# Kernel tuning notes

Measured on AMD Instinct MI355X. Metric: run time of the kernel, lower is better.

## Reference

```python
import jax, jax.numpy as jnp
import numpy as np

N_EMBD = 1024
N_HEAD = 16
HEAD_SIZE = 64


def setup_inputs() -> dict:
    key = jax.random.key(0)
    ks = jax.random.split(key, 6)
    B, T, C, H, D = 2, 2048, N_EMBD, N_HEAD, HEAD_SIZE
    s = 1.0 / np.sqrt(C)
    x = jax.random.normal(ks[0], (B, T, C), dtype=jnp.float32)
    Wq = jax.random.normal(ks[1], (H, C, D), dtype=jnp.float32) * s
    Wk = jax.random.normal(ks[2], (H, C, D), dtype=jnp.float32) * s
    Wv = jax.random.normal(ks[3], (H, C, D), dtype=jnp.float32) * s
    Wo = jax.random.normal(ks[4], (H * D, C), dtype=jnp.float32) * (1.0 / np.sqrt(H * D))
    bo = jax.random.normal(ks[5], (C,), dtype=jnp.float32) * 0.01
    return {"x": x, "Wq": Wq, "Wk": Wk, "Wv": Wv, "Wo": Wo, "bo": bo}


def reference(x, Wq, Wk, Wv, Wo, bo):
    B, T, C = x.shape
    H, _, D = Wq.shape
    # Per-head projections, batched across heads: [B,H,T,D]
    q = jnp.einsum('btc,hcd->bhtd', x, Wq)
    k = jnp.einsum('btc,hcd->bhtd', x, Wk)
    v = jnp.einsum('btc,hcd->bhtd', x, Wv)
    # NOTE: original scales by sqrt(C) = sqrt(n_embd), not sqrt(head_size)
    scale = 1.0 / jnp.sqrt(jnp.float32(C))
    att = jnp.einsum('bhtd,bhsd->bhts', q, k) * scale  # [B,H,T,T]
    causal = jnp.tril(jnp.ones((T, T), dtype=bool))
    att = jnp.where(causal, att, -jnp.inf)
    att = jax.nn.softmax(att, axis=-1)
    # dropout omitted (eval mode / deterministic reference)
    out = jnp.einsum('bhts,bhsd->bhtd', att, v)  # [B,H,T,D]
    out = out.transpose(0, 2, 1, 3).reshape(B, T, H * D)
    return out @ Wo + bo
```

## Files before the change

### kernel.cpp

```cpp
#include <hip/hip_runtime.h>
#include <hip/hip_bf16.h>


typedef __hip_bfloat16 bf16;
typedef __bf16 v8bf __attribute__((ext_vector_type(8)));
typedef float  v4f  __attribute__((ext_vector_type(4)));
typedef unsigned long long u64;
typedef unsigned int u32;

#define MFMA16(a, b, c) __builtin_amdgcn_mfma_f32_16x16x32_bf16((a), (b), (c), 0, 0, 0)

__device__ __forceinline__ bf16 f2b(float x) { return __float2bfloat16(x); }
__device__ __forceinline__ __bf16 f2braw(float x) {
  bf16 t = __float2bfloat16(x);
  return *reinterpret_cast<__bf16*>(&t);
}
__device__ __forceinline__ unsigned short f2bu(float x) {
  bf16 t = __float2bfloat16(x);
  return *reinterpret_cast<unsigned short*>(&t);
}

__device__ __forceinline__ void load16_lds(const bf16* gptr, const bf16* lptr) {
  __builtin_amdgcn_global_load_lds(
      (const __attribute__((address_space(1))) u32*)gptr,
      (__attribute__((address_space(3))) u32*)lptr, 16, 0, 0);
}

__global__ __launch_bounds__(256) void prep_kernel(
    const float* __restrict__ x,
    const float* __restrict__ Wq, const float* __restrict__ Wk,
    const float* __restrict__ Wv, const float* __restrict__ Wo,
    bf16* __restrict__ xb, bf16* __restrict__ wt, bf16* __restrict__ wot)
{
  __shared__ float Lt[32][33];
  const int bid = blockIdx.x, tid = threadIdx.x;

  if (bid < 2048) {
    size_t i = ((size_t)bid * 256 + tid) * 8;
    float4 f0 = *(const float4*)(x + i);
    float4 f1 = *(const float4*)(x + i + 4);
    v8bf v;
    v[0] = f2braw(f0.x); v[1] = f2braw(f0.y); v[2] = f2braw(f0.z); v[3] = f2braw(f0.w);
    v[4] = f2braw(f1.x); v[5] = f2braw(f1.y); v[6] = f2braw(f1.z); v[7] = f2braw(f1.w);
    *(v8bf*)(xb + i) = v;
    return;
  }
  const int tx = tid & 31, ty = tid >> 5;
  if (bid < 5120) {
    const int idx = bid - 2048;
    const int z = idx >> 6, rem = idx & 63;
    const int p = z >> 4, h = z & 15;
    const float* ib = ((p == 0) ? Wq : (p == 1) ? Wk : Wv) + (size_t)h * 65536;
    bf16* ob = wt + (size_t)z * 65536;
    const int j0 = (rem & 1) * 32, i0 = (rem >> 1) * 32;
    #pragma unroll
    for (int r = 0; r < 4; ++r)
      Lt[ty + 8 * r][tx] = ib[(size_t)(i0 + ty + 8 * r) * 64 + j0 + tx];
    __syncthreads();
    #pragma unroll
    for (int r = 0; r < 4; ++r)
      ob[(size_t)(j0 + ty + 8 * r) * 1024 + i0 + tx] = f2b(Lt[tx][ty + 8 * r]);
  } else {
    const int idx = bid - 5120;
    const int j0 = (idx & 31) * 32, i0 = (idx >> 5) * 32;
    #pragma unroll
    for (int r = 0; r < 4; ++r)
      Lt[ty + 8 * r][tx] = Wo[(size_t)(i0 + ty + 8 * r) * 1024 + j0 + tx];
    __syncthreads();
    #pragma unroll
    for (int r = 0; r < 4; ++r)
      wot[(size_t)(j0 + ty + 8 * r) * 1024 + i0 + tx] = f2b(Lt[tx][ty + 8 * r]);
  }
}

__global__ __launch_bounds__(256) void qkv_gemm_kernel(
    const bf16* __restrict__ xb, const bf16* __restrict__ wt,
    bf16* __restrict__ qkv)
{
  __shared__ __align__(16) bf16 Ash[2][128][32];
  __shared__ __align__(16) bf16 Bsh[2][128][32];

  const int mt = blockIdx.x, nt = blockIdx.y;
  const int tid = threadIdx.x, w = tid >> 6, lane = tid & 63;
  const int ln = lane & 15, quad = lane >> 4;
  const int wm = w >> 1, wn = w & 1;
  const int m0 = mt * 128, n0 = nt * 128;

  const v4f vzero = {0.f, 0.f, 0.f, 0.f};
  v4f acc[4][4];
  #pragma unroll
  for (int mf = 0; mf < 4; ++mf)
    #pragma unroll
    for (int nf = 0; nf < 4; ++nf) acc[mf][nf] = vzero;

  const int srow = lane >> 2, sseg = (lane & 3) * 8;
  const bf16* ga = xb + (size_t)(m0 + 32 * w + srow) * 1024 + sseg;
  const bf16* gb = wt + (size_t)(n0 + 32 * w + srow) * 1024 + sseg;

  {
    load16_lds(ga,             &Ash[0][32 * w][0]);
    load16_lds(ga + 16 * 1024, &Ash[0][32 * w + 16][0]);
    load16_lds(gb,             &Bsh[0][32 * w][0]);
    load16_lds(gb + 16 * 1024, &Bsh[0][32 * w + 16][0]);
  }

  for (int kt = 0; kt < 32; ++kt) {
    const int buf = kt & 1;
    __syncthreads();

    v8bf af[4], bfv[4];
    #pragma unroll
    for (int mf = 0; mf < 4; ++mf)
      af[mf] = *(const v8bf*)&Ash[buf][wm * 64 + mf * 16 + ln][quad * 8];
    #pragma unroll
    for (int nf = 0; nf < 4; ++nf)
      bfv[nf] = *(const v8bf*)&Bsh[buf][wn * 64 + nf * 16 + ln][quad * 8];

    if (kt < 31) {
      const int k0 = (kt + 1) * 32, nb = buf ^ 1;
      load16_lds(ga + k0,             &Ash[nb][32 * w][0]);
      load16_lds(ga + 16 * 1024 + k0, &Ash[nb][32 * w + 16][0]);
      load16_lds(gb + k0,             &Bsh[nb][32 * w][0]);
      load16_lds(gb + 16 * 1024 + k0, &Bsh[nb][32 * w + 16][0]);
    }

    #pragma unroll
    for (int mf = 0; mf < 4; ++mf)
      #pragma unroll
      for (int nf = 0; nf < 4; ++nf)
        acc[mf][nf] = MFMA16(af[mf], bfv[nf], acc[mf][nf]);
  }

  const int jcol0 = n0 + wn * 64;
  const int p = jcol0 >> 10;
  const int h = (jcol0 >> 6) & 15;
  const float scale = (p == 0) ? 0.0450841149f : 1.0f;

  if (p < 2) {
    bf16* base = qkv + (size_t)p * 4194304 + (size_t)h * 262144;
    #pragma unroll
    for (int mf = 0; mf < 4; ++mf)
      #pragma unroll
      for (int nf = 0; nf < 4; ++nf) {
        int d = nf * 16 + ln;
        #pragma unroll
        for (int r = 0; r < 4; ++r) {
          int m = m0 + wm * 64 + mf * 16 + quad * 4 + r;
          base[(size_t)m * 64 + d] = f2b(acc[mf][nf][r] * scale);
        }
      }
  } else {
    bf16* vb = qkv + (size_t)2 * 4194304 + (size_t)h * 262144;
    #pragma unroll
    for (int mf = 0; mf < 4; ++mf) {
      int mrow = m0 + wm * 64 + mf * 16 + quad * 4;
      int bi = mrow >> 11, t0 = mrow & 2047;
      #pragma unroll
      for (int nf = 0; nf < 4; ++nf) {
        int d = nf * 16 + ln;
        u64 pk = (u64)f2bu(acc[mf][nf][0]) |
                 ((u64)f2bu(acc[mf][nf][1]) << 16) |
                 ((u64)f2bu(acc[mf][nf][2]) << 32) |
                 ((u64)f2bu(acc[mf][nf][3]) << 48);
        *(u64*)(vb + (size_t)bi * 131072 + (size_t)d * 2048 + t0) = pk;
      }
    }
  }
}

__global__ __launch_bounds__(256, 4) void attn_kernel(
    const bf16* __restrict__ qkv, bf16* __restrict__ att)
{
  __shared__ __align__(16) bf16 Ksh[2][64][64];
  __shared__ __align__(16) bf16 Vsh[2][64][64];

  const int fid = blockIdx.x;
  const int j = fid >> 5;
  const int jr = j & 7, jq = j >> 3;
  const int mt = (jq == 0) ? (31 - jr) : (jq == 1) ? (8 + jr)
               : (jq == 2) ? (23 - jr) : jr;
  const int grp = fid & 31;
  const int b = grp >> 4, h = grp & 15;

  const int tid = threadIdx.x, w = tid >> 6, lane = tid & 63;
  const int ln = lane & 15, quad = lane >> 4;

  const bf16* qbase  = qkv + (size_t)h * 262144 + (size_t)b * 131072;
  const bf16* kbase  = qbase + 4194304;
  const bf16* vtbase = qbase + 8388608;

  const int l8 = lane & 7, r8 = lane >> 3;
  const int slot = l8 ^ r8;
  const int p0 = w * 16 + r8, p1 = p0 + 8;
  const int kp0 = (p0 & 32) | ((p0 & 12) << 1) | ((p0 & 16) >> 2) | (p0 & 3);
  const int kp1 = (p1 & 32) | ((p1 & 12) << 1) | ((p1 & 16) >> 2) | (p1 & 3);
  const bf16* gk0 = kbase + kp0 * 64 + slot * 8;
  const bf16* gk1 = kbase + kp1 * 64 + slot * 8;
  const bf16* gv0 = vtbase + p0 * 2048 + slot * 8;
  const bf16* gv1 = gv0 + 8 * 2048;

  const int sw = ln & 7;
  const int c0 = ((quad    ) ^ sw) * 8;
  const int c1 = ((quad + 4) ^ sw) * 8;
  const int rowoff = ln * 64;

  v8bf vone;
  {
    unsigned short u = 0x3F80;
    __bf16 e = *reinterpret_cast<__bf16*>(&u);
    #pragma unroll
    for (int jj = 0; jj < 8; ++jj) vone[jj] = e;
  }
  const v4f vzero = {0.f, 0.f, 0.f, 0.f};
  const float NEG = -30000.0f;

  #define STAGE(KB, BUF) {                                       \
    load16_lds(gk0 + (KB) * 4096, &Ksh[BUF][w * 16][0]);         \
    load16_lds(gk1 + (KB) * 4096, &Ksh[BUF][w * 16 + 8][0]);     \
    load16_lds(gv0 + (KB) * 64,   &Vsh[BUF][w * 16][0]);         \
    load16_lds(gv1 + (KB) * 64,   &Vsh[BUF][w * 16 + 8][0]); }

  const int wrow = mt * 64 + w * 16;
  const int qg = wrow + ln;

  v8bf aq[2];
  #pragma unroll
  for (int ks = 0; ks < 2; ++ks)
    aq[ks] = *(const v8bf*)(qbase + (size_t)(wrow + ln) * 64 + ks * 32 + quad * 8);

  v4f o[4], lacc;
  lacc = vzero;
  #pragma unroll
  for (int dt = 0; dt < 4; ++dt) o[dt] = vzero;

  STAGE(0, 0)

  const int kb_end = mt;
  for (int kb = 0; kb <= kb_end; ++kb) {
    const int buf = kb & 1;
    __syncthreads();

    v8bf kf[2][4], vf[2][4];
    const bf16* kr = &Ksh[buf][0][0];
    const bf16* vr = &Vsh[buf][0][0];
    #pragma unroll
    for (int nf = 0; nf < 4; ++nf) {
      kf[0][nf] = *(const v8bf*)(kr + nf * 1024 + rowoff + c0);
      kf[1][nf] = *(const v8bf*)(kr + nf * 1024 + rowoff + c1);
      vf[0][nf] = *(const v8bf*)(vr + nf * 1024 + rowoff + c0);
      vf[1][nf] = *(const v8bf*)(vr + nf * 1024 + rowoff + c1);
    }

    if (kb < kb_end) STAGE(kb + 1, buf ^ 1)

    __builtin_amdgcn_s_setprio(1);
    v4f s[4];
    #pragma unroll
    for (int nf = 0; nf < 4; ++nf) s[nf] = vzero;
    #pragma unroll
    for (int ks = 0; ks < 2; ++ks)
      #pragma unroll
      for (int nf = 0; nf < 4; ++nf)
        s[nf] = MFMA16(kf[ks][nf], aq[ks], s[nf]);
    __builtin_amdgcn_s_setprio(0);

    if (kb == kb_end) {
      #pragma unroll
      for (int nf = 0; nf < 4; ++nf) {
        const int kc = kb * 64 + (nf >> 1) * 32 + quad * 8 + (nf & 1) * 4;
        #pragma unroll
        for (int r = 0; r < 4; ++r)
          if (kc + r > qg) s[nf][r] = NEG;
      }
    }

    float ex[4][4];
    #pragma unroll
    for (int nf = 0; nf < 4; ++nf)
      #pragma unroll
      for (int r = 0; r < 4; ++r)
        ex[nf][r] = exp2f(s[nf][r]);

    union { u32 w[4]; v8bf v; } pu[2];
    #pragma unroll
    for (int ks = 0; ks < 2; ++ks)
      #pragma unroll
      for (int hh = 0; hh < 2; ++hh)
        #pragma unroll
        for (int wi = 0; wi < 2; ++wi)
          asm("v_cvt_pk_bf16_f32 %0, %1, %2"
              : "=v"(pu[ks].w[hh * 2 + wi])
              : "v"(ex[2 * ks + hh][2 * wi]), "v"(ex[2 * ks + hh][2 * wi + 1]));

    __builtin_amdgcn_s_setprio(1);
    lacc = MFMA16(pu[0].v, vone, lacc);
    lacc = MFMA16(pu[1].v, vone, lacc);
    #pragma unroll
    for (int ks = 0; ks < 2; ++ks)
      #pragma unroll
      for (int dt = 0; dt < 4; ++dt)
        o[dt] = MFMA16(pu[ks].v, vf[ks][dt], o[dt]);
    __builtin_amdgcn_s_setprio(0);
  }
  #undef STAGE

  v4f inv;
  #pragma unroll
  for (int r = 0; r < 4; ++r) inv[r] = 1.0f / lacc[r];
  #pragma unroll
  for (int dt = 0; dt < 4; ++dt)
    #pragma unroll
    for (int r = 0; r < 4; ++r) {
      int m = b * 2048 + wrow + quad * 4 + r;
      att[(size_t)m * 1024 + h * 64 + dt * 16 + ln] = f2b(o[dt][r] * inv[r]);
    }
}

__global__ __launch_bounds__(256) void out_gemm_kernel(
    const bf16* __restrict__ att, const bf16* __restrict__ wot,
    const float* __restrict__ bo, float* __restrict__ out)
{
  __shared__ __align__(16) bf16 Ash[2][128][32];
  __shared__ __align__(16) bf16 Bsh[2][64][32];

  const int mt = blockIdx.x, nt = blockIdx.y;
  const int tid = threadIdx.x, w = tid >> 6, lane = tid & 63;
  const int ln = lane & 15, quad = lane >> 4;
  const int wm = w >> 1, wn = w & 1;
  const int m0 = mt * 128, n0 = nt * 64;

  const v4f vzero = {0.f, 0.f, 0.f, 0.f};
  v4f acc[4][2];
  #pragma unroll
  for (int mf = 0; mf < 4; ++mf)
    #pragma unroll
    for (int nf = 0; nf < 2; ++nf) acc[mf][nf] = vzero;

  const int srow = lane >> 2, sseg = (lane & 3) * 8;
  const bf16* ga = att + (size_t)(m0 + 32 * w + srow) * 1024 + sseg;
  const bf16* gb = wot + (size_t)(n0 + 16 * w + srow) * 1024 + sseg;

  {
    load16_lds(ga,             &Ash[0][32 * w][0]);
    load16_lds(ga + 16 * 1024, &Ash[0][32 * w + 16][0]);
    load16_lds(gb,             &Bsh[0][16 * w][0]);
  }

  for (int kt = 0; kt < 32; ++kt) {
    const int buf = kt & 1;
    __syncthreads();

    v8bf af[4], bfv[2];
    #pragma unroll
    for (int mf = 0; mf < 4; ++mf)
      af[mf] = *(const v8bf*)&Ash[buf][wm * 64 + mf * 16 + ln][quad * 8];
    #pragma unroll
    for (int nf = 0; nf < 2; ++nf)
      bfv[nf] = *(const v8bf*)&Bsh[buf][wn * 32 + nf * 16 + ln][quad * 8];

    if (kt < 31) {
      const int k0 = (kt + 1) * 32, nb = buf ^ 1;
      load16_lds(ga + k0,             &Ash[nb][32 * w][0]);
      load16_lds(ga + 16 * 1024 + k0, &Ash[nb][32 * w + 16][0]);
      load16_lds(gb + k0,             &Bsh[nb][16 * w][0]);
    }

    #pragma unroll
    for (int mf = 0; mf < 4; ++mf)
      #pragma unroll
      for (int nf = 0; nf < 2; ++nf)
        acc[mf][nf] = MFMA16(af[mf], bfv[nf], acc[mf][nf]);
  }

  #pragma unroll
  for (int nf = 0; nf < 2; ++nf) {
    int j = n0 + wn * 32 + nf * 16 + ln;
    float bias = bo[j];
    #pragma unroll
    for (int mf = 0; mf < 4; ++mf)
      #pragma unroll
      for (int r = 0; r < 4; ++r) {
        int m = m0 + wm * 64 + mf * 16 + quad * 4 + r;
        out[(size_t)m * 1024 + j] = acc[mf][nf][r] + bias;
      }
  }
}

extern "C" void kernel_launch(void* const* d_in, const int* in_sizes, int n_in,
                              void* d_out, int out_size, void* d_ws, size_t ws_size,
                              hipStream_t stream) {
  const float* x  = (const float*)d_in[0];
  const float* Wq = (const float*)d_in[1];
  const float* Wk = (const float*)d_in[2];
  const float* Wv = (const float*)d_in[3];
  const float* Wo = (const float*)d_in[4];
  const float* bo = (const float*)d_in[5];
  float* out = (float*)d_out;

  bf16* xb  = (bf16*)d_ws;
  bf16* wt  = xb + 4194304;
  bf16* wot = xb + 7340032;
  bf16* qkv = xb + 8388608;
  bf16* att = xb + 20971520;

  prep_kernel<<<6144, 256, 0, stream>>>(x, Wq, Wk, Wv, Wo, xb, wt, wot);
  qkv_gemm_kernel<<<dim3(32, 24), 256, 0, stream>>>(xb, wt, qkv);
  attn_kernel<<<1024, 256, 0, stream>>>(qkv, att);
  out_gemm_kernel<<<dim3(32, 16), 256, 0, stream>>>(att, wot, bo, out);
}
```

Measured before the change: 168.7 us.

## Split attention key tile across wave pairs with LDS reduction of partial outputs

Changes the attention kernel's wave decomposition. Each wave now handles 32 query rows against half of each 64-key tile, instead of 16 query rows against the full tile. Each wave therefore loads half the K fragments and reuses its K and V fragments across two query chunks, which cuts LDS read traffic per MFMA. The partial outputs and row sums from the two key halves are combined at the end through an LDS union buffer, at the cost of an extra reduction phase, two more barriers and more accumulator registers.

```diff
diff --git a/kernel.cpp b/kernel.cpp
--- a/kernel.cpp
+++ b/kernel.cpp
@@ -171,8 +171,11 @@
 __global__ __launch_bounds__(256, 4) void attn_kernel(
     const bf16* __restrict__ qkv, bf16* __restrict__ att)
 {
-  __shared__ __align__(16) bf16 Ksh[2][64][64];
-  __shared__ __align__(16) bf16 Vsh[2][64][64];
+  union ShU {
+    struct { bf16 K[2][64][64]; bf16 V[2][64][64]; } t;
+    struct { float O[2][64][36]; float L[2][36]; } c;
+  };
+  __shared__ __align__(16) ShU sh;
 
   const int fid = blockIdx.x;
   const int j = fid >> 5;
@@ -184,6 +187,7 @@
 
   const int tid = threadIdx.x, w = tid >> 6, lane = tid & 63;
   const int ln = lane & 15, quad = lane >> 4;
+  const int qh = w & 1, kh = w >> 1;
 
   const bf16* qbase  = qkv + (size_t)h * 262144 + (size_t)b * 131072;
   const bf16* kbase  = qbase + 4194304;
@@ -200,9 +204,11 @@
   const bf16* gv1 = gv0 + 8 * 2048;
 
   const int sw = ln & 7;
-  const int c0 = ((quad    ) ^ sw) * 8;
-  const int c1 = ((quad + 4) ^ sw) * 8;
-  const int rowoff = ln * 64;
+  const int cc0 = ((quad    ) ^ sw) * 8;
+  const int cc1 = ((quad + 4) ^ sw) * 8;
+  const int cck = kh ? cc1 : cc0;
+  const int krow0 = (kh * 32 + ln) * 64;
+  const int krow1 = krow0 + 16 * 64;
 
   v8bf vone;
   {
@@ -215,23 +221,29 @@
   const float NEG = -30000.0f;
 
   #define STAGE(KB, BUF) {                                       \
-    load16_lds(gk0 + (KB) * 4096, &Ksh[BUF][w * 16][0]);         \
-    load16_lds(gk1 + (KB) * 4096, &Ksh[BUF][w * 16 + 8][0]);     \
-    load16_lds(gv0 + (KB) * 64,   &Vsh[BUF][w * 16][0]);         \
-    load16_lds(gv1 + (KB) * 64,   &Vsh[BUF][w * 16 + 8][0]); }
-
-  const int wrow = mt * 64 + w * 16;
-  const int qg = wrow + ln;
-
-  v8bf aq[2];
+    load16_lds(gk0 + (KB) * 4096, &sh.t.K[BUF][w * 16][0]);      \
+    load16_lds(gk1 + (KB) * 4096, &sh.t.K[BUF][w * 16 + 8][0]);  \
+    load16_lds(gv0 + (KB) * 64,   &sh.t.V[BUF][w * 16][0]);      \
+    load16_lds(gv1 + (KB) * 64,   &sh.t.V[BUF][w * 16 + 8][0]); }
+
+  const int row0 = mt * 64;
+  const int qrow = row0 + qh * 32;
+
+  v8bf aq[2][2];
   #pragma unroll
-  for (int ks = 0; ks < 2; ++ks)
-    aq[ks] = *(const v8bf*)(qbase + (size_t)(wrow + ln) * 64 + ks * 32 + quad * 8);
-
-  v4f o[4], lacc;
-  lacc = vzero;
+  for (int mc = 0; mc < 2; ++mc)
+    #pragma unroll
+    for (int ks = 0; ks < 2; ++ks)
+      aq[mc][ks] = *(const v8bf*)(qbase +
+          (size_t)(qrow + mc * 16 + ln) * 64 + ks * 32 + quad * 8);
+
+  v4f o[2][4], lacc[2];
   #pragma unroll
-  for (int dt = 0; dt < 4; ++dt) o[dt] = vzero;
+  for (int mc = 0; mc < 2; ++mc) {
+    lacc[mc] = vzero;
+    #pragma unroll
+    for (int dt = 0; dt < 4; ++dt) o[mc][dt] = vzero;
+  }
 
   STAGE(0, 0)
 
@@ -240,80 +252,99 @@
     const int buf = kb & 1;
     __syncthreads();
 
-    v8bf kf[2][4], vf[2][4];
-    const bf16* kr = &Ksh[buf][0][0];
-    const bf16* vr = &Vsh[buf][0][0];
-    #pragma unroll
-    for (int nf = 0; nf < 4; ++nf) {
-      kf[0][nf] = *(const v8bf*)(kr + nf * 1024 + rowoff + c0);
-      kf[1][nf] = *(const v8bf*)(kr + nf * 1024 + rowoff + c1);
-      vf[0][nf] = *(const v8bf*)(vr + nf * 1024 + rowoff + c0);
-      vf[1][nf] = *(const v8bf*)(vr + nf * 1024 + rowoff + c1);
-    }
+    v8bf kf[2][2], vf[4];
+    const bf16* kr = &sh.t.K[buf][0][0];
+    const bf16* vr = &sh.t.V[buf][0][0];
+    kf[0][0] = *(const v8bf*)(kr + krow0 + cc0);
+    kf[1][0] = *(const v8bf*)(kr + krow0 + cc1);
+    kf[0][1] = *(const v8bf*)(kr + krow1 + cc0);
+    kf[1][1] = *(const v8bf*)(kr + krow1 + cc1);
+    #pragma unroll
+    for (int dt = 0; dt < 4; ++dt)
+      vf[dt] = *(const v8bf*)(vr + (dt * 16 + ln) * 64 + cck);
 
     if (kb < kb_end) STAGE(kb + 1, buf ^ 1)
 
-    __builtin_amdgcn_s_setprio(1);
-    v4f s[4];
-    #pragma unroll
-    for (int nf = 0; nf < 4; ++nf) s[nf] = vzero;
-    #pragma unroll
-    for (int ks = 0; ks < 2; ++ks)
-      #pragma unroll
-      for (int nf = 0; nf < 4; ++nf)
-        s[nf] = MFMA16(kf[ks][nf], aq[ks], s[nf]);
-    __builtin_amdgcn_s_setprio(0);
-
-    if (kb == kb_end) {
-      #pragma unroll
-      for (int nf = 0; nf < 4; ++nf) {
-        const int kc = kb * 64 + (nf >> 1) * 32 + quad * 8 + (nf & 1) * 4;
+    #pragma unroll
+    for (int mc = 0; mc < 2; ++mc) {
+      __builtin_amdgcn_s_setprio(1);
+      v4f s[2];
+      s[0] = vzero; s[1] = vzero;
+      #pragma unroll
+      for (int ks = 0; ks < 2; ++ks)
+        #pragma unroll
+        for (int nfl = 0; nfl < 2; ++nfl)
+          s[nfl] = MFMA16(kf[ks][nfl], aq[mc][ks], s[nfl]);
+      __builtin_amdgcn_s_setprio(0);
+
+      const int qg = qrow + mc * 16 + ln;
+      if (kb == kb_end) {
+        #pragma unroll
+        for (int nfl = 0; nfl < 2; ++nfl) {
+          const int kc = kb * 64 + kh * 32 + quad * 8 + nfl * 4;
+          #pragma unroll
+          for (int r = 0; r < 4; ++r)
+            if (kc + r > qg) s[nfl][r] = NEG;
+        }
+      }
+
+      float ex[2][4];
+      #pragma unroll
+      for (int nfl = 0; nfl < 2; ++nfl)
         #pragma unroll
         for (int r = 0; r < 4; ++r)
-          if (kc + r > qg) s[nf][r] = NEG;
-      }
-    }
-
-    float ex[4][4];
-    #pragma unroll
-    for (int nf = 0; nf < 4; ++nf)
-      #pragma unroll
-      for (int r = 0; r < 4; ++r)
-        ex[nf][r] = exp2f(s[nf][r]);
-
-    union { u32 w[4]; v8bf v; } pu[2];
-    #pragma unroll
-    for (int ks = 0; ks < 2; ++ks)
-      #pragma unroll
-      for (int hh = 0; hh < 2; ++hh)
+          ex[nfl][r] = exp2f(s[nfl][r]);
+
+      union { u32 uw[4]; v8bf v; } pu;
+      #pragma unroll
+      for (int nfl = 0; nfl < 2; ++nfl)
         #pragma unroll
         for (int wi = 0; wi < 2; ++wi)
           asm("v_cvt_pk_bf16_f32 %0, %1, %2"
-              : "=v"(pu[ks].w[hh * 2 + wi])
-              : "v"(ex[2 * ks + hh][2 * wi]), "v"(ex[2 * ks + hh][2 * wi + 1]));
-
-    __builtin_amdgcn_s_setprio(1);
-    lacc = MFMA16(pu[0].v, vone, lacc);
-    lacc = MFMA16(pu[1].v, vone, lacc);
-    #pragma unroll
-    for (int ks = 0; ks < 2; ++ks)
+              : "=v"(pu.uw[nfl * 2 + wi])
+              : "v"(ex[nfl][2 * wi]), "v"(ex[nfl][2 * wi + 1]));
+
+      __builtin_amdgcn_s_setprio(1);
+      lacc[mc] = MFMA16(pu.v, vone, lacc[mc]);
       #pragma unroll
       for (int dt = 0; dt < 4; ++dt)
-        o[dt] = MFMA16(pu[ks].v, vf[ks][dt], o[dt]);
-    __builtin_amdgcn_s_setprio(0);
+        o[mc][dt] = MFMA16(pu.v, vf[dt], o[mc][dt]);
+      __builtin_amdgcn_s_setprio(0);
+    }
   }
   #undef STAGE
 
-  v4f inv;
-  #pragma unroll
-  for (int r = 0; r < 4; ++r) inv[r] = 1.0f / lacc[r];
-  #pragma unroll
-  for (int dt = 0; dt < 4; ++dt)
-    #pragma unroll
-    for (int r = 0; r < 4; ++r) {
-      int m = b * 2048 + wrow + quad * 4 + r;
-      att[(size_t)m * 1024 + h * 64 + dt * 16 + ln] = f2b(o[dt][r] * inv[r]);
-    }
+  __syncthreads();
+  if (kh == 1) {
+    #pragma unroll
+    for (int mc = 0; mc < 2; ++mc) {
+      #pragma unroll
+      for (int dt = 0; dt < 4; ++dt)
+        *(v4f*)&sh.c.O[qh][dt * 16 + ln][mc * 16 + quad * 4] = o[mc][dt];
+      if (ln == 0)
+        *(v4f*)&sh.c.L[qh][mc * 16 + quad * 4] = lacc[mc];
+    }
+  }
+  __syncthreads();
+  if (kh == 0) {
+    #pragma unroll
+    for (int mc = 0; mc < 2; ++mc) {
+      v4f pl = *(const v4f*)&sh.c.L[qh][mc * 16 + quad * 4];
+      v4f inv;
+      #pragma unroll
+      for (int r = 0; r < 4; ++r) inv[r] = 1.0f / (lacc[mc][r] + pl[r]);
+      #pragma unroll
+      for (int dt = 0; dt < 4; ++dt) {
+        v4f po = *(const v4f*)&sh.c.O[qh][dt * 16 + ln][mc * 16 + quad * 4];
+        #pragma unroll
+        for (int r = 0; r < 4; ++r) {
+          int m = b * 2048 + qrow + mc * 16 + quad * 4 + r;
+          att[(size_t)m * 1024 + h * 64 + dt * 16 + ln] =
+              f2b((o[mc][dt][r] + po[r]) * inv[r]);
+        }
+      }
+    }
+  }
 }
 
 __global__ __launch_bounds__(256) void out_gemm_kernel(
```

Result: faster. 164.3 us (-2.6%).
